# Kernel optimization log

Measured on AMD Instinct MI355X. Metric: run time of the kernel, lower is better.

## Reference

```python
import jax, jax.numpy as jnp
import numpy as np
import math

B, S, D, H = 4, 2048, 1024, 16
HD = D // H  # 64


def setup_inputs() -> dict:
    key = jax.random.key(0)
    ks = jax.random.split(key, 12)
    s_in = 1.0 / math.sqrt(D)
    inp = {
        "x_v": jax.random.normal(ks[0], (B, S, D), jnp.float32),
        "x_k": jax.random.normal(ks[1], (B, S, D), jnp.float32),
        "x_q": jax.random.normal(ks[2], (B, S, D), jnp.float32),
        "mask": jax.random.randint(ks[3], (B, S, S), 0, 2, jnp.int32),
        "Wq": jax.random.normal(ks[4], (H, D, HD), jnp.float32) * s_in,
        "bq": jax.random.normal(ks[5], (H, HD), jnp.float32) * s_in,
        "Wk": jax.random.normal(ks[6], (H, D, HD), jnp.float32) * s_in,
        "bk": jax.random.normal(ks[7], (H, HD), jnp.float32) * s_in,
        "Wv": jax.random.normal(ks[8], (H, D, HD), jnp.float32) * s_in,
        "bv": jax.random.normal(ks[9], (H, HD), jnp.float32) * s_in,
        "Wo": jax.random.normal(ks[10], (D, D), jnp.float32) * s_in,
        "bo": jax.random.normal(ks[11], (D,), jnp.float32) * s_in,
    }
    return inp


def reference(x_v, x_k, x_q, mask, Wq, bq, Wk, bk, Wv, bv, Wo, bo):
    # Batched per-head projections: [B,S,D] x [H,D,E] -> [B,H,S,E]
    q = jnp.einsum("bsd,hde->bhse", x_q, Wq) + bq[None, :, None, :]
    k = jnp.einsum("bsd,hde->bhse", x_k, Wk) + bk[None, :, None, :]
    v = jnp.einsum("bsd,hde->bhse", x_v, Wv) + bv[None, :, None, :]
    scale = 1.0 / math.sqrt(HD)
    scores = jnp.einsum("bhqe,bhke->bhqk", q, k) * scale  # [B,H,Sq,Sk]
    # Faithful to original: masked positions are set to 0 (not -inf) BEFORE softmax
    scores = jnp.where(mask[:, None, :, :] == 0, 0.0, scores)
    attn = jax.nn.softmax(scores, axis=-1)
    z = jnp.einsum("bhqk,bhke->bhqe", attn, v)  # [B,H,Sq,E]
    # Concat over heads in head order (matches torch.cat along dim=2)
    z = z.transpose(0, 2, 1, 3).reshape(B, S, D)
    return z @ Wo + bo
```

## Files before the change

kernel.cpp:

```cpp
#include <hip/hip_runtime.h>

typedef unsigned short u16;
typedef unsigned long long u64;
typedef __attribute__((ext_vector_type(8))) short bf16x8;
typedef __attribute__((ext_vector_type(4))) float f32x4;

#define LD 72
#define C_SCALE 0.18033688011112043f

__device__ __forceinline__ u16 f2b(float x) {
  union { float f; unsigned u; } c; c.f = x;
  unsigned r = (c.u + 0x7fffu + ((c.u >> 16) & 1u)) >> 16;
  return (u16)r;
}

__device__ __forceinline__ unsigned pk2(float a, float b) {
#if __has_builtin(__builtin_amdgcn_cvt_pk_bf16_f32)
  typedef __attribute__((ext_vector_type(2))) __bf16 b2;
  b2 r = __builtin_amdgcn_cvt_pk_bf16_f32(a, b);
  union { b2 v; unsigned u; } c; c.v = r;
  return c.u;
#else
  union { float f; unsigned u; } x, y;
  x.f = a; y.f = b;
  return ((x.u + 0x8000u) >> 16) | ((y.u + 0x8000u) & 0xffff0000u);
#endif
}

__device__ __forceinline__ void gll16(const u16* g, u16* l) {
  __builtin_amdgcn_global_load_lds(
      (const __attribute__((address_space(1))) void*)g,
      (__attribute__((address_space(3))) void*)l, 16, 0, 0);
}

__global__ __launch_bounds__(256) void cvt_bf16(
    const float4* __restrict__ src, ushort4* __restrict__ dst, int n4) {
  int stride = gridDim.x * 256;
  for (int i = blockIdx.x * 256 + threadIdx.x; i < n4; i += stride) {
    float4 v = src[i];
    ushort4 o = { f2b(v.x), f2b(v.y), f2b(v.z), f2b(v.w) };
    dst[i] = o;
  }
}

__global__ __launch_bounds__(256) void transpose_cvt(
    const float* __restrict__ src, u16* __restrict__ dst, int R, int C) {
  __shared__ u16 tile[64][65];
  const size_t mo = (size_t)blockIdx.z * R * C;
  const float* s = src + mo;
  u16* d = dst + mo;
  const int r0 = blockIdx.x * 64, c0 = blockIdx.y * 64;
  const int t = threadIdx.x;
#pragma unroll
  for (int rep = 0; rep < 16; ++rep) {
    int idx = rep * 256 + t;
    int i = idx >> 6, j = idx & 63;
    tile[j][i] = f2b(s[(size_t)(r0 + i) * C + c0 + j]);
  }
  __syncthreads();
#pragma unroll
  for (int rep = 0; rep < 16; ++rep) {
    int idx = rep * 256 + t;
    int jj = idx >> 6, ii = idx & 63;
    d[(size_t)(c0 + jj) * R + r0 + ii] = tile[jj][ii];
  }
}

__global__ __launch_bounds__(256) void pack_mask(
    const int* __restrict__ m, u64* __restrict__ mp) {
  const int nw = (gridDim.x * 256) >> 6;
  const int wid = (blockIdx.x * 256 + threadIdx.x) >> 6;
  const int lane = threadIdx.x & 63;
  const int total = 4 * 2048 * 32;
  for (int i = wid; i < total; i += nw) {
    int v = m[(size_t)i * 64 + lane];
    u64 bits = __ballot(v != 0);
    if (lane == 0) mp[i] = bits;
  }
}

template <int MODE>
__global__ __launch_bounds__(256, 2) void gemm_t(
    const u16* __restrict__ A, const u16* __restrict__ W,
    const float* __restrict__ bias, void* __restrict__ outp, float scale) {
  __shared__ u16 S[17408];
  u16* Asm = S;
  u16* Bsm = S + 8192;
  const int s0 = blockIdx.x * 128, n0 = blockIdx.y * 128;
  const int t = threadIdx.x, wv = t >> 6, lane = t & 63;
  const int m16 = lane & 15, q4 = lane >> 4;
  const int rsub = lane >> 3, csub = lane & 7;
  const int wr = (wv & 1) * 64, wc = (wv >> 1) * 64;
  f32x4 acc[4][4];
#pragma unroll
  for (int i = 0; i < 4; ++i)
#pragma unroll
    for (int j = 0; j < 4; ++j) acc[i][j] = (f32x4){0.f, 0.f, 0.f, 0.f};

  for (int k0 = 0; k0 < 1024; k0 += 64) {
    __syncthreads();
#pragma unroll
    for (int i = 0; i < 4; ++i) {
      int chunk = wv * 4 + i;
      gll16(A + (size_t)(s0 + chunk * 8 + rsub) * 1024 + k0 + csub * 8,
            Asm + chunk * 512 + lane * 8);
      gll16(W + (size_t)(n0 + chunk * 8 + rsub) * 1024 + k0 + csub * 8,
            Bsm + chunk * 512 + lane * 8);
    }
    __syncthreads();
#pragma unroll
    for (int ks = 0; ks < 2; ++ks) {
      bf16x8 af[4], bfr[4];
#pragma unroll
      for (int i = 0; i < 4; ++i)
        af[i] = *(const bf16x8*)(Asm + (wr + i * 16 + m16) * 64 + ks * 32 + q4 * 8);
#pragma unroll
      for (int j = 0; j < 4; ++j)
        bfr[j] = *(const bf16x8*)(Bsm + (wc + j * 16 + m16) * 64 + ks * 32 + q4 * 8);
#pragma unroll
      for (int i = 0; i < 4; ++i)
#pragma unroll
        for (int j = 0; j < 4; ++j)
          acc[i][j] = __builtin_amdgcn_mfma_f32_16x16x32_bf16(af[i], bfr[j], acc[i][j], 0, 0, 0);
    }
  }

  if (MODE == 0) {
    u16* out = (u16*)outp;
#pragma unroll
    for (int j = 0; j < 4; ++j) {
      int n = n0 + wc + j * 16 + m16;
      int h = n >> 6, e = n & 63;
      float bval = bias[n];
#pragma unroll
      for (int i = 0; i < 4; ++i)
#pragma unroll
        for (int r = 0; r < 4; ++r) {
          int s = s0 + wr + i * 16 + q4 * 4 + r;
          int bi = s >> 11, sl = s & 2047;
          out[((size_t)(bi * 16 + h) * 2048 + sl) * 64 + e] =
              f2b((acc[i][j][r] + bval) * scale);
        }
    }
  } else if (MODE == 2) {
    float* out = (float*)outp;
#pragma unroll
    for (int j = 0; j < 4; ++j) {
      int n = n0 + wc + j * 16 + m16;
      float bval = bias[n];
#pragma unroll
      for (int i = 0; i < 4; ++i)
#pragma unroll
        for (int r = 0; r < 4; ++r) {
          int s = s0 + wr + i * 16 + q4 * 4 + r;
          out[(size_t)s * 1024 + n] = acc[i][j][r] + bval;
        }
    }
  } else {
    __syncthreads();
#pragma unroll
    for (int j = 0; j < 4; ++j) {
      int nl = wc + j * 16 + m16;
      float bval = bias[n0 + nl];
#pragma unroll
      for (int i = 0; i < 4; ++i)
#pragma unroll
        for (int r = 0; r < 4; ++r)
          S[nl * 136 + wr + i * 16 + q4 * 4 + r] = f2b(acc[i][j][r] + bval);
    }
    __syncthreads();
    u16* vt = (u16*)outp;
    const int bi = s0 >> 11, sl0 = s0 & 2047;
#pragma unroll
    for (int rep = 0; rep < 8; ++rep) {
      int u = rep * 256 + t;
      int rr = u >> 4, cc = (u & 15) * 8;
      int n = n0 + rr, h = n >> 6, e = n & 63;
      *(int4*)(vt + ((size_t)(bi * 16 + h) * 64 + e) * 2048 + sl0 + cc) =
          *(const int4*)(S + rr * 136 + cc);
    }
  }
}

__global__ __launch_bounds__(256, 4) void attn(
    const u16* __restrict__ qb, const u16* __restrict__ kb,
    const u16* __restrict__ vt, const u64* __restrict__ mp,
    u16* __restrict__ zb) {
  __shared__ u16 Kl[2][64 * LD];
  __shared__ u16 Vl[2][64 * LD];
  const int id = blockIdx.x;
  const int qi = id >> 6;
  const int bh = id & 63;
  const int b = bh >> 4, h = bh & 15;
  const int t = threadIdx.x, w = t >> 6, lane = t & 63;
  const int m16 = lane & 15, q4 = lane >> 4;
  const size_t bho = (size_t)bh * 2048;
  const u16* qp = qb + bho * 64;
  const u16* kp = kb + bho * 64;
  const u16* vp = vt + bho * 64;
  const int qbase = qi * 128 + w * 32;

  bf16x8 qa[2][2];
#pragma unroll
  for (int qg = 0; qg < 2; ++qg)
#pragma unroll
    for (int ks = 0; ks < 2; ++ks)
      qa[qg][ks] = *(const bf16x8*)(qp + (size_t)(qbase + qg * 16 + m16) * 64 + ks * 32 + q4 * 8);

  f32x4 oacc[2][4], lacc[2];
#pragma unroll
  for (int qg = 0; qg < 2; ++qg) {
    lacc[qg] = (f32x4){0.f, 0.f, 0.f, 0.f};
#pragma unroll
    for (int g = 0; g < 4; ++g) oacc[qg][g] = (f32x4){0.f, 0.f, 0.f, 0.f};
  }
  bf16x8 ones;
#pragma unroll
  for (int j = 0; j < 8; ++j) ones[j] = (short)0x3f80;

  const u64* mpq0 = mp + ((size_t)b * 2048 + qbase + m16) * 32;
  const u64* mpq1 = mp + ((size_t)b * 2048 + qbase + 16 + m16) * 32;

  const int ch = t & 7, rw = t >> 3;
  const int sK = (((rw >> 2) & 1) * 16) + (((rw >> 3) & 3) * 4) + (rw & 3);

  int4 pk0 = *(const int4*)(kp + (size_t)rw * 64 + ch * 8);
  int4 pk1 = *(const int4*)(kp + (size_t)(rw + 32) * 64 + ch * 8);
  int4 pv0 = *(const int4*)(vp + (size_t)rw * 2048 + ch * 8);
  int4 pv1 = *(const int4*)(vp + (size_t)(rw + 32) * 2048 + ch * 8);
  *(int4*)(&Kl[0][sK * LD + ch * 8]) = pk0;
  *(int4*)(&Kl[0][(sK + 32) * LD + ch * 8]) = pk1;
  *(int4*)(&Vl[0][rw * LD + ch * 8]) = pv0;
  *(int4*)(&Vl[0][(rw + 32) * LD + ch * 8]) = pv1;
  __syncthreads();

  for (int kt = 0; kt < 32; ++kt) {
    const int cur = kt & 1;
    if (kt < 31) {
      const int k0n = (kt + 1) * 64;
      pk0 = *(const int4*)(kp + (size_t)(k0n + rw) * 64 + ch * 8);
      pk1 = *(const int4*)(kp + (size_t)(k0n + rw + 32) * 64 + ch * 8);
      pv0 = *(const int4*)(vp + (size_t)rw * 2048 + k0n + ch * 8);
      pv1 = *(const int4*)(vp + (size_t)(rw + 32) * 2048 + k0n + ch * 8);
    }
    const u64 mb0 = mpq0[kt];
    const u64 mb1 = mpq1[kt];

#pragma unroll
    for (int bb = 0; bb < 2; ++bb) {
      bf16x8 kf00 = *(const bf16x8*)(&Kl[cur][(bb * 32 + m16) * LD + q4 * 8]);
      bf16x8 kf01 = *(const bf16x8*)(&Kl[cur][(bb * 32 + m16) * LD + 32 + q4 * 8]);
      bf16x8 kf10 = *(const bf16x8*)(&Kl[cur][(bb * 32 + 16 + m16) * LD + q4 * 8]);
      bf16x8 kf11 = *(const bf16x8*)(&Kl[cur][(bb * 32 + 16 + m16) * LD + 32 + q4 * 8]);
      const unsigned by0 = (unsigned)(mb0 >> (bb * 32 + q4 * 8)) & 0xFFu;
      const unsigned by1 = (unsigned)(mb1 >> (bb * 32 + q4 * 8)) & 0xFFu;
      bf16x8 pa[2];
#pragma unroll
      for (int qg = 0; qg < 2; ++qg) {
        f32x4 sa = (f32x4){0.f, 0.f, 0.f, 0.f};
        f32x4 sb = (f32x4){0.f, 0.f, 0.f, 0.f};
        sa = __builtin_amdgcn_mfma_f32_16x16x32_bf16(kf00, qa[qg][0], sa, 0, 0, 0);
        sa = __builtin_amdgcn_mfma_f32_16x16x32_bf16(kf01, qa[qg][1], sa, 0, 0, 0);
        sb = __builtin_amdgcn_mfma_f32_16x16x32_bf16(kf10, qa[qg][0], sb, 0, 0, 0);
        sb = __builtin_amdgcn_mfma_f32_16x16x32_bf16(kf11, qa[qg][1], sb, 0, 0, 0);
        const unsigned by = qg ? by1 : by0;
        float p[8];
#pragma unroll
        for (int r = 0; r < 4; ++r) {
          p[r] = __builtin_amdgcn_exp2f((by & (1u << r)) ? sa[r] : 0.f);
          p[4 + r] = __builtin_amdgcn_exp2f((by & (1u << (4 + r))) ? sb[r] : 0.f);
        }
        union { unsigned u[4]; bf16x8 v; } pu;
        pu.u[0] = pk2(p[0], p[1]);
        pu.u[1] = pk2(p[2], p[3]);
        pu.u[2] = pk2(p[4], p[5]);
        pu.u[3] = pk2(p[6], p[7]);
        pa[qg] = pu.v;
        lacc[qg] = __builtin_amdgcn_mfma_f32_16x16x32_bf16(pa[qg], ones, lacc[qg], 0, 0, 0);
      }
#pragma unroll
      for (int e = 0; e < 4; ++e) {
        bf16x8 vf = *(const bf16x8*)(&Vl[cur][(e * 16 + m16) * LD + bb * 32 + q4 * 8]);
        oacc[0][e] = __builtin_amdgcn_mfma_f32_16x16x32_bf16(pa[0], vf, oacc[0][e], 0, 0, 0);
        oacc[1][e] = __builtin_amdgcn_mfma_f32_16x16x32_bf16(pa[1], vf, oacc[1][e], 0, 0, 0);
      }
    }

    if (kt < 31) {
      const int nxt = cur ^ 1;
      *(int4*)(&Kl[nxt][sK * LD + ch * 8]) = pk0;
      *(int4*)(&Kl[nxt][(sK + 32) * LD + ch * 8]) = pk1;
      *(int4*)(&Vl[nxt][rw * LD + ch * 8]) = pv0;
      *(int4*)(&Vl[nxt][(rw + 32) * LD + ch * 8]) = pv1;
      __syncthreads();
    }
  }

#pragma unroll
  for (int qg = 0; qg < 2; ++qg) {
#pragma unroll
    for (int r = 0; r < 4; ++r) {
      float inv = 1.f / lacc[qg][r];
      size_t zr = ((size_t)b * 2048 + qbase + qg * 16 + q4 * 4 + r) * 1024 + h * 64;
#pragma unroll
      for (int e = 0; e < 4; ++e) {
        zb[zr + e * 16 + m16] = f2b(oacc[qg][e][r] * inv);
      }
    }
  }
}

extern "C" void kernel_launch(void* const* d_in, const int* in_sizes, int n_in,
                              void* d_out, int out_size, void* d_ws, size_t ws_size,
                              hipStream_t stream) {
  const float* x_v = (const float*)d_in[0];
  const float* x_k = (const float*)d_in[1];
  const float* x_q = (const float*)d_in[2];
  const int* mask = (const int*)d_in[3];
  const float* Wq = (const float*)d_in[4];
  const float* bq = (const float*)d_in[5];
  const float* Wk = (const float*)d_in[6];
  const float* bk = (const float*)d_in[7];
  const float* Wv = (const float*)d_in[8];
  const float* bv = (const float*)d_in[9];
  const float* Wo = (const float*)d_in[10];
  const float* bo = (const float*)d_in[11];
  float* out = (float*)d_out;

  char* ws = (char*)d_ws;
  size_t off = 0;
  auto alloc_u16 = [&](size_t n) {
    u16* p = (u16*)(ws + off);
    off += n * sizeof(u16);
    return p;
  };
  u16* wq_t = alloc_u16((size_t)16 * 64 * 1024);
  u16* wk_t = alloc_u16((size_t)16 * 64 * 1024);
  u16* wv_t = alloc_u16((size_t)16 * 64 * 1024);
  u16* wo_t = alloc_u16((size_t)1024 * 1024);
  u16* qb = alloc_u16((size_t)8192 * 1024);
  u16* kb = alloc_u16((size_t)8192 * 1024);
  u16* vtb = alloc_u16((size_t)8192 * 1024);
  u16* xq16 = alloc_u16((size_t)8192 * 1024);
  u16* xk16 = alloc_u16((size_t)8192 * 1024);
  u16* xv16 = alloc_u16((size_t)8192 * 1024);
  u64* mp = (u64*)(ws + off);
  off += (size_t)262144 * 8;
  u16* zb = xq16;

  transpose_cvt<<<dim3(16, 1, 16), 256, 0, stream>>>(Wq, wq_t, 1024, 64);
  transpose_cvt<<<dim3(16, 1, 16), 256, 0, stream>>>(Wk, wk_t, 1024, 64);
  transpose_cvt<<<dim3(16, 1, 16), 256, 0, stream>>>(Wv, wv_t, 1024, 64);
  transpose_cvt<<<dim3(16, 16, 1), 256, 0, stream>>>(Wo, wo_t, 1024, 1024);
  pack_mask<<<dim3(1024), 256, 0, stream>>>(mask, mp);
  const int n4 = 8192 * 1024 / 4;
  cvt_bf16<<<dim3(1024), 256, 0, stream>>>((const float4*)x_q, (ushort4*)xq16, n4);
  cvt_bf16<<<dim3(1024), 256, 0, stream>>>((const float4*)x_k, (ushort4*)xk16, n4);
  cvt_bf16<<<dim3(1024), 256, 0, stream>>>((const float4*)x_v, (ushort4*)xv16, n4);
  gemm_t<0><<<dim3(64, 8), 256, 0, stream>>>(xq16, wq_t, bq, qb, C_SCALE);
  gemm_t<0><<<dim3(64, 8), 256, 0, stream>>>(xk16, wk_t, bk, kb, 1.0f);
  gemm_t<1><<<dim3(64, 8), 256, 0, stream>>>(xv16, wv_t, bv, vtb, 1.0f);
  attn<<<dim3(1024), 256, 0, stream>>>(qb, kb, vtb, mp, zb);
  gemm_t<2><<<dim3(64, 8), 256, 0, stream>>>(zb, wo_t, bo, out, 1.0f);
}
```

Baseline: 448.8 us.

## Batch weight/input conversions and QKV GEMMs into single launches; prefetch mask bits

Merges the four weight transposes into one launch, the three input bf16 conversions into one 2D-grid launch, and the three QKV projection GEMMs into one launch that picks its operands by blockIdx.z. This cuts launch count and lets independent blocks fill the GPU together, for example 1536 GEMM blocks instead of three serial waves of 512. In the attention kernel, the packed mask words for the next key tile are loaded alongside the K/V prefetch, so the mask load latency is not exposed at the start of each tile. The cost is a few runtime selects on blockIdx and slightly more register pressure in attention.

```diff
diff --git a/kernel.cpp b/kernel.cpp
--- a/kernel.cpp
+++ b/kernel.cpp
@@ -33,8 +33,13 @@
       (__attribute__((address_space(3))) void*)l, 16, 0, 0);
 }
 
-__global__ __launch_bounds__(256) void cvt_bf16(
-    const float4* __restrict__ src, ushort4* __restrict__ dst, int n4) {
+__global__ __launch_bounds__(256) void cvt_bf16_3(
+    const float4* __restrict__ s0, const float4* __restrict__ s1,
+    const float4* __restrict__ s2, ushort4* __restrict__ d0,
+    ushort4* __restrict__ d1, ushort4* __restrict__ d2, int n4) {
+  const int z = blockIdx.y;
+  const float4* src = z == 0 ? s0 : z == 1 ? s1 : s2;
+  ushort4* dst = z == 0 ? d0 : z == 1 ? d1 : d2;
   int stride = gridDim.x * 256;
   for (int i = blockIdx.x * 256 + threadIdx.x; i < n4; i += stride) {
     float4 v = src[i];
@@ -43,13 +48,28 @@
   }
 }
 
-__global__ __launch_bounds__(256) void transpose_cvt(
-    const float* __restrict__ src, u16* __restrict__ dst, int R, int C) {
+__global__ __launch_bounds__(256) void transpose_cvt_all(
+    const float* __restrict__ Wq, const float* __restrict__ Wk,
+    const float* __restrict__ Wv, const float* __restrict__ Wo,
+    u16* __restrict__ wq_t, u16* __restrict__ wk_t,
+    u16* __restrict__ wv_t, u16* __restrict__ wo_t) {
   __shared__ u16 tile[64][65];
-  const size_t mo = (size_t)blockIdx.z * R * C;
-  const float* s = src + mo;
-  u16* d = dst + mo;
-  const int r0 = blockIdx.x * 64, c0 = blockIdx.y * 64;
+  const int id = blockIdx.x;
+  const int which = id >> 8, sub = id & 255;
+  const float* s;
+  u16* d;
+  int R, C, r0, c0;
+  if (which < 3) {
+    const float* W = which == 0 ? Wq : which == 1 ? Wk : Wv;
+    u16* D = which == 0 ? wq_t : which == 1 ? wk_t : wv_t;
+    int h = sub >> 4, rt = sub & 15;
+    s = W + (size_t)h * 1024 * 64;
+    d = D + (size_t)h * 64 * 1024;
+    R = 1024; C = 64; r0 = rt * 64; c0 = 0;
+  } else {
+    s = Wo; d = wo_t;
+    R = 1024; C = 1024; r0 = ((sub >> 4) & 15) * 64; c0 = (sub & 15) * 64;
+  }
   const int t = threadIdx.x;
 #pragma unroll
   for (int rep = 0; rep < 16; ++rep) {
@@ -79,24 +99,12 @@
   }
 }
 
-template <int MODE>
-__global__ __launch_bounds__(256, 2) void gemm_t(
+__device__ __forceinline__ void gemm_core(
     const u16* __restrict__ A, const u16* __restrict__ W,
-    const float* __restrict__ bias, void* __restrict__ outp, float scale) {
-  __shared__ u16 S[17408];
-  u16* Asm = S;
-  u16* Bsm = S + 8192;
-  const int s0 = blockIdx.x * 128, n0 = blockIdx.y * 128;
-  const int t = threadIdx.x, wv = t >> 6, lane = t & 63;
-  const int m16 = lane & 15, q4 = lane >> 4;
+    u16* Asm, u16* Bsm, int s0, int n0, int wv, int lane,
+    int m16, int q4, f32x4 acc[4][4]) {
   const int rsub = lane >> 3, csub = lane & 7;
   const int wr = (wv & 1) * 64, wc = (wv >> 1) * 64;
-  f32x4 acc[4][4];
-#pragma unroll
-  for (int i = 0; i < 4; ++i)
-#pragma unroll
-    for (int j = 0; j < 4; ++j) acc[i][j] = (f32x4){0.f, 0.f, 0.f, 0.f};
-
   for (int k0 = 0; k0 < 1024; k0 += 64) {
     __syncthreads();
 #pragma unroll
@@ -124,9 +132,37 @@
           acc[i][j] = __builtin_amdgcn_mfma_f32_16x16x32_bf16(af[i], bfr[j], acc[i][j], 0, 0, 0);
     }
   }
-
-  if (MODE == 0) {
-    u16* out = (u16*)outp;
+}
+
+__global__ __launch_bounds__(256, 2) void qkv_gemm(
+    const u16* __restrict__ xq, const u16* __restrict__ xk,
+    const u16* __restrict__ xv, const u16* __restrict__ wq,
+    const u16* __restrict__ wk, const u16* __restrict__ wv_,
+    const float* __restrict__ bq, const float* __restrict__ bk,
+    const float* __restrict__ bv, u16* __restrict__ qb,
+    u16* __restrict__ kb, u16* __restrict__ vtb) {
+  __shared__ u16 S[17408];
+  u16* Asm = S;
+  u16* Bsm = S + 8192;
+  const int z = blockIdx.z;
+  const u16* A = z == 0 ? xq : z == 1 ? xk : xv;
+  const u16* W = z == 0 ? wq : z == 1 ? wk : wv_;
+  const float* bias = z == 0 ? bq : z == 1 ? bk : bv;
+  const int s0 = blockIdx.x * 128, n0 = blockIdx.y * 128;
+  const int t = threadIdx.x, wvi = t >> 6, lane = t & 63;
+  const int m16 = lane & 15, q4 = lane >> 4;
+  const int wr = (wvi & 1) * 64, wc = (wvi >> 1) * 64;
+  f32x4 acc[4][4];
+#pragma unroll
+  for (int i = 0; i < 4; ++i)
+#pragma unroll
+    for (int j = 0; j < 4; ++j) acc[i][j] = (f32x4){0.f, 0.f, 0.f, 0.f};
+
+  gemm_core(A, W, Asm, Bsm, s0, n0, wvi, lane, m16, q4, acc);
+
+  if (z < 2) {
+    u16* out = z == 0 ? qb : kb;
+    const float scale = z == 0 ? C_SCALE : 1.0f;
 #pragma unroll
     for (int j = 0; j < 4; ++j) {
       int n = n0 + wc + j * 16 + m16;
@@ -142,20 +178,6 @@
               f2b((acc[i][j][r] + bval) * scale);
         }
     }
-  } else if (MODE == 2) {
-    float* out = (float*)outp;
-#pragma unroll
-    for (int j = 0; j < 4; ++j) {
-      int n = n0 + wc + j * 16 + m16;
-      float bval = bias[n];
-#pragma unroll
-      for (int i = 0; i < 4; ++i)
-#pragma unroll
-        for (int r = 0; r < 4; ++r) {
-          int s = s0 + wr + i * 16 + q4 * 4 + r;
-          out[(size_t)s * 1024 + n] = acc[i][j][r] + bval;
-        }
-    }
   } else {
     __syncthreads();
 #pragma unroll
@@ -169,16 +191,47 @@
           S[nl * 136 + wr + i * 16 + q4 * 4 + r] = f2b(acc[i][j][r] + bval);
     }
     __syncthreads();
-    u16* vt = (u16*)outp;
     const int bi = s0 >> 11, sl0 = s0 & 2047;
 #pragma unroll
     for (int rep = 0; rep < 8; ++rep) {
       int u = rep * 256 + t;
       int rr = u >> 4, cc = (u & 15) * 8;
       int n = n0 + rr, h = n >> 6, e = n & 63;
-      *(int4*)(vt + ((size_t)(bi * 16 + h) * 64 + e) * 2048 + sl0 + cc) =
+      *(int4*)(vtb + ((size_t)(bi * 16 + h) * 64 + e) * 2048 + sl0 + cc) =
           *(const int4*)(S + rr * 136 + cc);
     }
+  }
+}
+
+__global__ __launch_bounds__(256, 2) void out_gemm(
+    const u16* __restrict__ Z, const u16* __restrict__ Wot,
+    const float* __restrict__ bo, float* __restrict__ out) {
+  __shared__ u16 S[17408];
+  u16* Asm = S;
+  u16* Bsm = S + 8192;
+  const int s0 = blockIdx.x * 128, n0 = blockIdx.y * 128;
+  const int t = threadIdx.x, wvi = t >> 6, lane = t & 63;
+  const int m16 = lane & 15, q4 = lane >> 4;
+  const int wr = (wvi & 1) * 64, wc = (wvi >> 1) * 64;
+  f32x4 acc[4][4];
+#pragma unroll
+  for (int i = 0; i < 4; ++i)
+#pragma unroll
+    for (int j = 0; j < 4; ++j) acc[i][j] = (f32x4){0.f, 0.f, 0.f, 0.f};
+
+  gemm_core(Z, Wot, Asm, Bsm, s0, n0, wvi, lane, m16, q4, acc);
+
+#pragma unroll
+  for (int j = 0; j < 4; ++j) {
+    int n = n0 + wc + j * 16 + m16;
+    float bval = bo[n];
+#pragma unroll
+    for (int i = 0; i < 4; ++i)
+#pragma unroll
+      for (int r = 0; r < 4; ++r) {
+        int s = s0 + wr + i * 16 + q4 * 4 + r;
+        out[(size_t)s * 1024 + n] = acc[i][j][r] + bval;
+      }
   }
 }
 
@@ -228,6 +281,7 @@
   int4 pk1 = *(const int4*)(kp + (size_t)(rw + 32) * 64 + ch * 8);
   int4 pv0 = *(const int4*)(vp + (size_t)rw * 2048 + ch * 8);
   int4 pv1 = *(const int4*)(vp + (size_t)(rw + 32) * 2048 + ch * 8);
+  u64 mb0 = mpq0[0], mb1 = mpq1[0];
   *(int4*)(&Kl[0][sK * LD + ch * 8]) = pk0;
   *(int4*)(&Kl[0][(sK + 32) * LD + ch * 8]) = pk1;
   *(int4*)(&Vl[0][rw * LD + ch * 8]) = pv0;
@@ -236,15 +290,16 @@
 
   for (int kt = 0; kt < 32; ++kt) {
     const int cur = kt & 1;
+    u64 nmb0, nmb1;
     if (kt < 31) {
       const int k0n = (kt + 1) * 64;
       pk0 = *(const int4*)(kp + (size_t)(k0n + rw) * 64 + ch * 8);
       pk1 = *(const int4*)(kp + (size_t)(k0n + rw + 32) * 64 + ch * 8);
       pv0 = *(const int4*)(vp + (size_t)rw * 2048 + k0n + ch * 8);
       pv1 = *(const int4*)(vp + (size_t)(rw + 32) * 2048 + k0n + ch * 8);
-    }
-    const u64 mb0 = mpq0[kt];
-    const u64 mb1 = mpq1[kt];
+      nmb0 = mpq0[kt + 1];
+      nmb1 = mpq1[kt + 1];
+    }
 
 #pragma unroll
     for (int bb = 0; bb < 2; ++bb) {
@@ -292,6 +347,8 @@
       *(int4*)(&Kl[nxt][(sK + 32) * LD + ch * 8]) = pk1;
       *(int4*)(&Vl[nxt][rw * LD + ch * 8]) = pv0;
       *(int4*)(&Vl[nxt][(rw + 32) * LD + ch * 8]) = pv1;
+      mb0 = nmb0;
+      mb1 = nmb1;
       __syncthreads();
     }
   }
@@ -348,18 +405,15 @@
   off += (size_t)262144 * 8;
   u16* zb = xq16;
 
-  transpose_cvt<<<dim3(16, 1, 16), 256, 0, stream>>>(Wq, wq_t, 1024, 64);
-  transpose_cvt<<<dim3(16, 1, 16), 256, 0, stream>>>(Wk, wk_t, 1024, 64);
-  transpose_cvt<<<dim3(16, 1, 16), 256, 0, stream>>>(Wv, wv_t, 1024, 64);
-  transpose_cvt<<<dim3(16, 16, 1), 256, 0, stream>>>(Wo, wo_t, 1024, 1024);
+  transpose_cvt_all<<<dim3(1024), 256, 0, stream>>>(
+      Wq, Wk, Wv, Wo, wq_t, wk_t, wv_t, wo_t);
   pack_mask<<<dim3(1024), 256, 0, stream>>>(mask, mp);
   const int n4 = 8192 * 1024 / 4;
-  cvt_bf16<<<dim3(1024), 256, 0, stream>>>((const float4*)x_q, (ushort4*)xq16, n4);
-  cvt_bf16<<<dim3(1024), 256, 0, stream>>>((const float4*)x_k, (ushort4*)xk16, n4);
-  cvt_bf16<<<dim3(1024), 256, 0, stream>>>((const float4*)x_v, (ushort4*)xv16, n4);
-  gemm_t<0><<<dim3(64, 8), 256, 0, stream>>>(xq16, wq_t, bq, qb, C_SCALE);
-  gemm_t<0><<<dim3(64, 8), 256, 0, stream>>>(xk16, wk_t, bk, kb, 1.0f);
-  gemm_t<1><<<dim3(64, 8), 256, 0, stream>>>(xv16, wv_t, bv, vtb, 1.0f);
+  cvt_bf16_3<<<dim3(512, 3), 256, 0, stream>>>(
+      (const float4*)x_q, (const float4*)x_k, (const float4*)x_v,
+      (ushort4*)xq16, (ushort4*)xk16, (ushort4*)xv16, n4);
+  qkv_gemm<<<dim3(64, 8, 3), 256, 0, stream>>>(
+      xq16, xk16, xv16, wq_t, wk_t, wv_t, bq, bk, bv, qb, kb, vtb);
   attn<<<dim3(1024), 256, 0, stream>>>(qb, kb, vtb, mp, zb);
-  gemm_t<2><<<dim3(64, 8), 256, 0, stream>>>(zb, wo_t, bo, out, 1.0f);
-}
+  out_gemm<<<dim3(64, 8), 256, 0, stream>>>(zb, wo_t, bo, out);
+}
```

Result: faster. 420.7 us (-6.3%).
